# Performance work log

Measured on AMD Instinct MI355X. Metric: run time of the kernel, lower is better.

Reference implementation:

```python
import jax, jax.numpy as jnp
import numpy as np

B = 1_000_000
NBOX = 6


def setup_inputs() -> dict:
    key = jax.random.key(0)
    k1, k2, k3 = jax.random.split(key, 3)
    # midpoint-format boxes: positive w/h, coords in [0,1)-ish
    pred = jax.random.uniform(k1, (B, NBOX, 4), dtype=jnp.float32)
    truth = jax.random.uniform(k2, (B, NBOX, 4), dtype=jnp.float32)
    invalid = jax.random.uniform(k3, (B, NBOX)) < 0.2  # [B,6]
    truth = jnp.where(invalid[..., None], jnp.float32(-1.0), truth)
    return {"pred": pred, "truth": truth}


def _iou_midpoint(p, t):
    # p, t: [..., 4] in (cx, cy, w, h) format
    p_x1 = p[..., 0] - p[..., 2] / 2
    p_y1 = p[..., 1] - p[..., 3] / 2
    p_x2 = p[..., 0] + p[..., 2] / 2
    p_y2 = p[..., 1] + p[..., 3] / 2
    t_x1 = t[..., 0] - t[..., 2] / 2
    t_y1 = t[..., 1] - t[..., 3] / 2
    t_x2 = t[..., 0] + t[..., 2] / 2
    t_y2 = t[..., 1] + t[..., 3] / 2
    x1 = jnp.maximum(p_x1, t_x1)
    y1 = jnp.maximum(p_y1, t_y1)
    x2 = jnp.minimum(p_x2, t_x2)
    y2 = jnp.minimum(p_y2, t_y2)
    inter = jnp.clip(x2 - x1, 0) * jnp.clip(y2 - y1, 0)
    area_p = jnp.abs((p_x2 - p_x1) * (p_y2 - p_y1))
    area_t = jnp.abs((t_x2 - t_x1) * (t_y2 - t_y1))
    return inter / (area_p + area_t - inter + 1e-6)


def reference(pred, truth):
    # valid box: truth row is not the sentinel [-1,-1,-1,-1]
    valid = ~jnp.all(truth == -1.0, axis=-1)          # [B, 6] bool
    iou = _iou_midpoint(pred, truth)                   # [B, 6]
    vf = valid.astype(iou.dtype)
    total = jnp.sum(iou * vf)
    n_valid = jnp.sum(vf)
    mean_iou = jnp.where(n_valid > 0, total / jnp.maximum(n_valid, 1.0), 0.0)
    # original accumulates (1,1)-shaped iou tensors -> result shape (1,1)
    return mean_iou.reshape(1, 1)
```

## Files before the change

kernel.cpp:

```cpp
#include <hip/hip_runtime.h>


#define BLOCKS 1953
#define THREADS 256

typedef float vfloat4 __attribute__((ext_vector_type(4)));

__device__ __forceinline__ vfloat4 nt_load4(const float4* p) {
    return __builtin_nontemporal_load((const vfloat4*)p);
}

__device__ __forceinline__ void iou_accum(vfloat4 p, vfloat4 t,
                                          float& s_iou, float& s_cnt) {
    float v = (t.x == -1.0f && t.y == -1.0f &&
               t.z == -1.0f && t.w == -1.0f) ? 0.0f : 1.0f;

    float p_x1 = p.x - p.z * 0.5f;
    float p_y1 = p.y - p.w * 0.5f;
    float p_x2 = p.x + p.z * 0.5f;
    float p_y2 = p.y + p.w * 0.5f;
    float t_x1 = t.x - t.z * 0.5f;
    float t_y1 = t.y - t.w * 0.5f;
    float t_x2 = t.x + t.z * 0.5f;
    float t_y2 = t.y + t.w * 0.5f;

    float x1 = fmaxf(p_x1, t_x1);
    float y1 = fmaxf(p_y1, t_y1);
    float x2 = fminf(p_x2, t_x2);
    float y2 = fminf(p_y2, t_y2);

    float inter  = fmaxf(x2 - x1, 0.0f) * fmaxf(y2 - y1, 0.0f);
    float area_p = fabsf((p_x2 - p_x1) * (p_y2 - p_y1));
    float area_t = fabsf((t_x2 - t_x1) * (t_y2 - t_y1));

    float denom = area_p + area_t - inter + 1e-6f;
    s_iou += v * inter * __builtin_amdgcn_rcpf(denom);
    s_cnt += v;
}

__global__ __launch_bounds__(THREADS) void iou_partial(
    const float4* __restrict__ pred,
    const float4* __restrict__ truth,
    float* __restrict__ partials,
    int n)
{
    int tid = blockIdx.x * THREADS + threadIdx.x;
    const int stride = BLOCKS * THREADS;

    float s_iou0 = 0.0f, s_cnt0 = 0.0f;
    float s_iou1 = 0.0f, s_cnt1 = 0.0f;

    int i = tid;
    for (; i + 5 * stride < n; i += 6 * stride) {
        vfloat4 p0 = nt_load4(&pred[i]);
        vfloat4 p1 = nt_load4(&pred[i + stride]);
        vfloat4 p2 = nt_load4(&pred[i + 2 * stride]);
        vfloat4 p3 = nt_load4(&pred[i + 3 * stride]);
        vfloat4 p4 = nt_load4(&pred[i + 4 * stride]);
        vfloat4 p5 = nt_load4(&pred[i + 5 * stride]);
        vfloat4 t0 = nt_load4(&truth[i]);
        vfloat4 t1 = nt_load4(&truth[i + stride]);
        vfloat4 t2 = nt_load4(&truth[i + 2 * stride]);
        vfloat4 t3 = nt_load4(&truth[i + 3 * stride]);
        vfloat4 t4 = nt_load4(&truth[i + 4 * stride]);
        vfloat4 t5 = nt_load4(&truth[i + 5 * stride]);
        iou_accum(p0, t0, s_iou0, s_cnt0);
        iou_accum(p1, t1, s_iou1, s_cnt1);
        iou_accum(p2, t2, s_iou0, s_cnt0);
        iou_accum(p3, t3, s_iou1, s_cnt1);
        iou_accum(p4, t4, s_iou0, s_cnt0);
        iou_accum(p5, t5, s_iou1, s_cnt1);
    }
    for (; i < n; i += stride) {
        vfloat4 p = nt_load4(&pred[i]);
        vfloat4 t = nt_load4(&truth[i]);
        iou_accum(p, t, s_iou0, s_cnt0);
    }

    float s_iou = s_iou0 + s_iou1;
    float s_cnt = s_cnt0 + s_cnt1;

    for (int off = 32; off > 0; off >>= 1) {
        s_iou += __shfl_down(s_iou, off, 64);
        s_cnt += __shfl_down(s_cnt, off, 64);
    }

    __shared__ float lds_iou[THREADS / 64];
    __shared__ float lds_cnt[THREADS / 64];
    int lane = threadIdx.x & 63;
    int wave = threadIdx.x >> 6;
    if (lane == 0) {
        lds_iou[wave] = s_iou;
        lds_cnt[wave] = s_cnt;
    }
    __syncthreads();

    if (threadIdx.x == 0) {
        float a = 0.0f, b = 0.0f;
        #pragma unroll
        for (int w = 0; w < THREADS / 64; ++w) {
            a += lds_iou[w];
            b += lds_cnt[w];
        }
        partials[2 * blockIdx.x]     = a;
        partials[2 * blockIdx.x + 1] = b;
    }
}

__global__ __launch_bounds__(THREADS) void iou_finalize(
    const float* __restrict__ partials, int nblocks, float* __restrict__ out)
{
    float s_iou = 0.0f;
    float s_cnt = 0.0f;
    for (int i = threadIdx.x; i < nblocks; i += blockDim.x) {
        s_iou += partials[2 * i];
        s_cnt += partials[2 * i + 1];
    }
    for (int off = 32; off > 0; off >>= 1) {
        s_iou += __shfl_down(s_iou, off, 64);
        s_cnt += __shfl_down(s_cnt, off, 64);
    }
    __shared__ float lds_iou[THREADS / 64];
    __shared__ float lds_cnt[THREADS / 64];
    int lane = threadIdx.x & 63;
    int wave = threadIdx.x >> 6;
    if (lane == 0) {
        lds_iou[wave] = s_iou;
        lds_cnt[wave] = s_cnt;
    }
    __syncthreads();
    if (threadIdx.x == 0) {
        float a = 0.0f, b = 0.0f;
        #pragma unroll
        for (int w = 0; w < THREADS / 64; ++w) {
            a += lds_iou[w];
            b += lds_cnt[w];
        }
        out[0] = (b > 0.0f) ? (a / fmaxf(b, 1.0f)) : 0.0f;
    }
}

extern "C" void kernel_launch(void* const* d_in, const int* in_sizes, int n_in,
                              void* d_out, int out_size, void* d_ws, size_t ws_size,
                              hipStream_t stream) {
    const float4* pred  = (const float4*)d_in[0];
    const float4* truth = (const float4*)d_in[1];
    float* out = (float*)d_out;
    float* partials = (float*)d_ws;

    int n_pairs = in_sizes[0] / 4;

    iou_partial<<<BLOCKS, THREADS, 0, stream>>>(pred, truth, partials, n_pairs);
    iou_finalize<<<1, THREADS, 0, stream>>>(partials, BLOCKS, out);
}
```

Measured before the change: 190.6 us.

## Switch to contiguous per-block chunks with 8-way unroll and fewer blocks

Changes the work split from a grid-stride layout to contiguous per-block chunks, where each block walks its own range with 8 loads in flight per thread. The block count drops from 1953 to 1024, and the finalize kernel still reduces exactly BLOCKS partials. The aim is better DRAM locality and more memory-level parallelism per wave. The cost is fewer blocks resident on the GPU, and chunk boundaries that do not align with 256 leave a per-block remainder loop.

After: 188.8 us. No clear change (-1.0%).

```diff
diff --git a/kernel.cpp b/kernel.cpp
--- a/kernel.cpp
+++ b/kernel.cpp
@@ -1,8 +1,9 @@
 #include <hip/hip_runtime.h>
 
 
-#define BLOCKS 1953
+#define BLOCKS 1024
 #define THREADS 256
+#define UNROLL 8
 
 typedef float vfloat4 __attribute__((ext_vector_type(4)));
 
@@ -44,34 +45,41 @@
     float* __restrict__ partials,
     int n)
 {
-    int tid = blockIdx.x * THREADS + threadIdx.x;
-    const int stride = BLOCKS * THREADS;
+    const int chunk = (n + BLOCKS - 1) / BLOCKS;
+    const int base  = blockIdx.x * chunk;
+    const int end   = min(base + chunk, n);
 
     float s_iou0 = 0.0f, s_cnt0 = 0.0f;
     float s_iou1 = 0.0f, s_cnt1 = 0.0f;
 
-    int i = tid;
-    for (; i + 5 * stride < n; i += 6 * stride) {
+    int i = base + threadIdx.x;
+    for (; i + (UNROLL - 1) * THREADS < end; i += UNROLL * THREADS) {
         vfloat4 p0 = nt_load4(&pred[i]);
-        vfloat4 p1 = nt_load4(&pred[i + stride]);
-        vfloat4 p2 = nt_load4(&pred[i + 2 * stride]);
-        vfloat4 p3 = nt_load4(&pred[i + 3 * stride]);
-        vfloat4 p4 = nt_load4(&pred[i + 4 * stride]);
-        vfloat4 p5 = nt_load4(&pred[i + 5 * stride]);
+        vfloat4 p1 = nt_load4(&pred[i + 1 * THREADS]);
+        vfloat4 p2 = nt_load4(&pred[i + 2 * THREADS]);
+        vfloat4 p3 = nt_load4(&pred[i + 3 * THREADS]);
+        vfloat4 p4 = nt_load4(&pred[i + 4 * THREADS]);
+        vfloat4 p5 = nt_load4(&pred[i + 5 * THREADS]);
+        vfloat4 p6 = nt_load4(&pred[i + 6 * THREADS]);
+        vfloat4 p7 = nt_load4(&pred[i + 7 * THREADS]);
         vfloat4 t0 = nt_load4(&truth[i]);
-        vfloat4 t1 = nt_load4(&truth[i + stride]);
-        vfloat4 t2 = nt_load4(&truth[i + 2 * stride]);
-        vfloat4 t3 = nt_load4(&truth[i + 3 * stride]);
-        vfloat4 t4 = nt_load4(&truth[i + 4 * stride]);
-        vfloat4 t5 = nt_load4(&truth[i + 5 * stride]);
+        vfloat4 t1 = nt_load4(&truth[i + 1 * THREADS]);
+        vfloat4 t2 = nt_load4(&truth[i + 2 * THREADS]);
+        vfloat4 t3 = nt_load4(&truth[i + 3 * THREADS]);
+        vfloat4 t4 = nt_load4(&truth[i + 4 * THREADS]);
+        vfloat4 t5 = nt_load4(&truth[i + 5 * THREADS]);
+        vfloat4 t6 = nt_load4(&truth[i + 6 * THREADS]);
+        vfloat4 t7 = nt_load4(&truth[i + 7 * THREADS]);
         iou_accum(p0, t0, s_iou0, s_cnt0);
         iou_accum(p1, t1, s_iou1, s_cnt1);
         iou_accum(p2, t2, s_iou0, s_cnt0);
         iou_accum(p3, t3, s_iou1, s_cnt1);
         iou_accum(p4, t4, s_iou0, s_cnt0);
         iou_accum(p5, t5, s_iou1, s_cnt1);
+        iou_accum(p6, t6, s_iou0, s_cnt0);
+        iou_accum(p7, t7, s_iou1, s_cnt1);
     }
-    for (; i < n; i += stride) {
+    for (; i < end; i += THREADS) {
         vfloat4 p = nt_load4(&pred[i]);
         vfloat4 t = nt_load4(&truth[i]);
         iou_accum(p, t, s_iou0, s_cnt0);
```
